# Kernel optimization log

Measured on AMD Instinct MI355X. Metric: run time of the kernel, lower is better.

## Reference

```python
import jax, jax.numpy as jnp
import numpy as np

# ---- fixed 22-node graph from the module's build_graph (clique expansion of adj_list) ----
_ADJ_LIST = [[0, 2, 5, 8, 11], [0, 1, 4, 7, 10], [0, 3, 6, 9, 12, 15],
             [9, 14, 17, 19, 21], [9, 13, 16, 18, 20]]
_N = max(max(s) for s in _ADJ_LIST) + 1  # 22
_A = np.zeros((_N, _N), dtype=np.float32)
for s in _ADJ_LIST:
    for i in range(len(s)):
        for j in range(i + 1, len(s)):
            _A[s[i], s[j]] = 1.0
            _A[s[j], s[i]] = 1.0
_deg = _A.sum(axis=1)
_dinv = 1.0 / np.sqrt(np.maximum(_deg, 1.0))
A_HAT = jnp.asarray(_dinv[:, None] * _A * _dinv[None, :])  # D^{-1/2} A D^{-1/2}, DGL norm='both'

SEQ_LEN = 100
HID = 3


def setup_inputs() -> dict:
    key = jax.random.key(0)
    ks = jax.random.split(key, 9)
    B, IN = 16384, 32
    s_in = 1.0 / np.sqrt(IN)
    s_h = 1.0 / np.sqrt(HID)
    return {
        "x": jax.random.normal(ks[0], (B, IN), jnp.float32),
        "w_r_W": jax.random.normal(ks[1], (IN, HID), jnp.float32) * s_in,
        "w_r_b": jax.random.normal(ks[2], (HID,), jnp.float32) * s_in,
        "w_z_W": jax.random.normal(ks[3], (IN, HID), jnp.float32) * s_in,
        "w_z_b": jax.random.normal(ks[4], (HID,), jnp.float32) * s_in,
        "w_h_W": jax.random.normal(ks[5], (IN, HID), jnp.float32) * s_in,
        "w_h_b": jax.random.normal(ks[6], (HID,), jnp.float32) * s_in,
        "gcn_W": jax.random.normal(ks[7], (HID, HID), jnp.float32) * s_h,
        "gcn_b": jax.random.normal(ks[8], (HID,), jnp.float32) * s_h,
    }


def reference(x, w_r_W, w_r_b, w_z_W, w_z_b, w_h_W, w_h_b, gcn_W, gcn_b):
    B = x.shape[0]
    # input projections are constant across timesteps and nodes -> compute once, broadcast
    xr = (x @ w_r_W + w_r_b)[:, None, :]  # (B,1,H)
    xz = (x @ w_z_W + w_z_b)[:, None, :]
    xh = (x @ w_h_W + w_h_b)[:, None, :]

    def step(h, _):
        # GraphConv: symmetric-normalized aggregation, then linear + bias
        gh = jnp.einsum('nm,bmh->bnh', A_HAT, h) @ gcn_W + gcn_b  # (B,N,H)
        r = jax.nn.sigmoid(xr + gh)
        z = jax.nn.sigmoid(xz + gh)
        h_tilde = jnp.tanh(xh + r * gh)
        h_new = (1.0 - z) * h + z * h_tilde
        return h_new, h_new

    h0 = jnp.zeros((B, _N, HID), x.dtype)
    _, hs = jax.lax.scan(step, h0, None, length=SEQ_LEN)  # (T,B,N,H)
    out = jnp.transpose(hs, (1, 0, 2, 3)).reshape(B, -1)  # (B, T*N*H)
    return out
```

## Files before the change

### kernel.cpp

```cpp
#include <hip/hip_runtime.h>


#define TPB 64
#define REP 4
#define RPW 16
#define NGRP (16384 / TPB)
#define GRID (NGRP * REP)
#define T_TOTAL 100
#define SCH 10
#define NCHUNK (T_TOTAL / SCH)
#define ROW_F4 (SCH * 66 / 4)
#define STG_STRIDE (SCH * 9 + 1)
#define STG_SZ (TPB * STG_STRIDE)
#define F4_PER_REP (RPW * ROW_F4)
#define GITERS ((F4_PER_REP + TPB - 1) / TPB)

#if __has_builtin(__builtin_amdgcn_exp2f)
#define EXP2F __builtin_amdgcn_exp2f
#else
#define EXP2F exp2f
#endif
#if __has_builtin(__builtin_amdgcn_rcpf)
#define RCPF __builtin_amdgcn_rcpf
#else
#define RCPF(x) (1.0f / (x))
#endif

static __device__ __forceinline__ float fast_sigmoid(float x) {
    float e = EXP2F(-1.44269504f * x);
    return RCPF(1.0f + e);
}
static __device__ __forceinline__ float fast_tanh(float x) {
    float e = EXP2F(2.88539008f * x);
    return 1.0f - 2.0f * RCPF(1.0f + e);
}

__global__ __launch_bounds__(TPB) void gcgru_kernel(
    const float* __restrict__ x,
    const float* __restrict__ w_r_W, const float* __restrict__ w_r_b,
    const float* __restrict__ w_z_W, const float* __restrict__ w_z_b,
    const float* __restrict__ w_h_W, const float* __restrict__ w_h_b,
    const float* __restrict__ gcn_W, const float* __restrict__ gcn_b,
    float* __restrict__ out)
{
    __shared__ float wS[297];
    __shared__ float gwS[9];
    __shared__ float gbS[3];
    __shared__ unsigned int tabS[ROW_F4];
    __shared__ float stage[STG_SZ];

    const int tid = threadIdx.x;
    const int rep = blockIdx.x & (REP - 1);
    const int b0  = (blockIdx.x >> 2) * TPB;
    const int row0 = rep * RPW;

    for (int i = tid; i < 96; i += TPB) {
        wS[i]       = w_r_W[i];
        wS[96 + i]  = w_z_W[i];
        wS[192 + i] = w_h_W[i];
    }
    if (tid < 3) {
        wS[288 + tid] = w_r_b[tid];
        wS[291 + tid] = w_z_b[tid];
        wS[294 + tid] = w_h_b[tid];
        gbS[tid] = gcn_b[tid];
    }
    if (tid < 9) gwS[tid] = gcn_W[tid];
    {
        static const unsigned char cls3[66] = {
            0,1,2, 3,4,5, 3,4,5, 6,7,8, 3,4,5, 3,4,5, 6,7,8, 3,4,5, 3,4,5,
            0,1,2, 3,4,5, 3,4,5, 6,7,8, 3,4,5, 3,4,5, 6,7,8, 3,4,5, 3,4,5,
            3,4,5, 3,4,5, 3,4,5, 3,4,5
        };
        for (int j4 = tid; j4 < ROW_F4; j4 += TPB) {
            unsigned int w = 0;
            #pragma unroll
            for (int u = 0; u < 4; ++u) {
                int jj = 4 * j4 + u;
                int tl = jj / 66;
                int k  = jj - 66 * tl;
                w |= (unsigned int)(tl * 9 + cls3[k]) << (8 * u);
            }
            tabS[j4] = w;
        }
    }

    float xv[32];
    {
        const float4* xp = reinterpret_cast<const float4*>(x + (size_t)(b0 + tid) * 32);
        #pragma unroll
        for (int i = 0; i < 8; ++i) {
            float4 v = xp[i];
            xv[4*i+0] = v.x; xv[4*i+1] = v.y; xv[4*i+2] = v.z; xv[4*i+3] = v.w;
        }
    }
    float xr[3], xz[3], xh[3];
    #pragma unroll
    for (int j = 0; j < 3; ++j) { xr[j] = wS[288+j]; xz[j] = wS[291+j]; xh[j] = wS[294+j]; }
    #pragma unroll
    for (int i = 0; i < 32; ++i) {
        float xi = xv[i];
        #pragma unroll
        for (int j = 0; j < 3; ++j) {
            xr[j] = fmaf(xi, wS[i*3+j],       xr[j]);
            xz[j] = fmaf(xi, wS[96 + i*3+j],  xz[j]);
            xh[j] = fmaf(xi, wS[192 + i*3+j], xh[j]);
        }
    }

    float W9[9], gb3[3];
    #pragma unroll
    for (int i = 0; i < 9; ++i) W9[i] = gwS[i];
    #pragma unroll
    for (int j = 0; j < 3; ++j) gb3[j] = gbS[j];

    const float M00 = 0.0769230769f;
    const float M01 = 1.1094003925f;
    const float M02 = 0.4961389384f;
    const float M10 = 0.1386750491f;
    const float M11 = 0.75f;
    const float M20 = 0.2480694691f;
    const float M22 = 0.6f;

    float h[9];
    #pragma unroll
    for (int i = 0; i < 9; ++i) h[i] = 0.0f;

    float4* out4 = reinterpret_cast<float4*>(out);

    for (int chunk = 0; chunk < NCHUNK; ++chunk) {
        float* stw = stage + tid * STG_STRIDE;

        #pragma unroll
        for (int s = 0; s < SCH; ++s) {
            float mh[9], gh[9];
            #pragma unroll
            for (int j = 0; j < 3; ++j) {
                mh[j]     = M00 * h[j] + M01 * h[3+j] + M02 * h[6+j];
                mh[3 + j] = M10 * h[j] + M11 * h[3+j];
                mh[6 + j] = M20 * h[j] + M22 * h[6+j];
            }
            #pragma unroll
            for (int c = 0; c < 3; ++c)
                #pragma unroll
                for (int j = 0; j < 3; ++j)
                    gh[c*3+j] = gb3[j] + mh[c*3+0]*W9[j] + mh[c*3+1]*W9[3+j] + mh[c*3+2]*W9[6+j];
            #pragma unroll
            for (int c = 0; c < 3; ++c) {
                #pragma unroll
                for (int j = 0; j < 3; ++j) {
                    float g  = gh[c*3+j];
                    float r  = fast_sigmoid(xr[j] + g);
                    float z  = fast_sigmoid(xz[j] + g);
                    float ht = fast_tanh(xh[j] + r * g);
                    float hv = h[c*3+j];
                    h[c*3+j] = hv + z * (ht - hv);
                }
            }
            #pragma unroll
            for (int q = 0; q < 9; ++q) stw[s*9 + q] = h[q];
        }


        const int cbase = chunk * ROW_F4;
        for (int i = 0; i < GITERS; ++i) {
            int f = i * TPB + tid;
            if (f < F4_PER_REP) {
                int rl = f / ROW_F4;
                int j4 = f - rl * ROW_F4;
                int r  = row0 + rl;
                unsigned int tw = tabS[j4];
                const float* row = stage + r * STG_STRIDE;
                float4 v;
                v.x = row[tw & 255u];
                v.y = row[(tw >> 8)  & 255u];
                v.z = row[(tw >> 16) & 255u];
                v.w = row[tw >> 24];
                out4[(size_t)(b0 + r) * 1650 + cbase + j4] = v;
            }
        }
    }
}

extern "C" void kernel_launch(void* const* d_in, const int* in_sizes, int n_in,
                              void* d_out, int out_size, void* d_ws, size_t ws_size,
                              hipStream_t stream) {
    const float* xp     = (const float*)d_in[0];
    const float* w_r_W  = (const float*)d_in[1];
    const float* w_r_b  = (const float*)d_in[2];
    const float* w_z_W  = (const float*)d_in[3];
    const float* w_z_b  = (const float*)d_in[4];
    const float* w_h_W  = (const float*)d_in[5];
    const float* w_h_b  = (const float*)d_in[6];
    const float* gcn_W  = (const float*)d_in[7];
    const float* gcn_b  = (const float*)d_in[8];
    float* outp = (float*)d_out;

    gcgru_kernel<<<GRID, TPB, 0, stream>>>(xp, w_r_W, w_r_b, w_z_W, w_z_b,
                                           w_h_W, w_h_b, gcn_W, gcn_b, outp);
}
```

Baseline: 497.7 us.

## Split into compact-state compute kernel and separate gather-expand kernel via workspace

The fused kernel is split in two when enough workspace is available. The first kernel runs the recurrence once per batch row, with no 4x replication, and writes a compact padded 12-float record per timestep to workspace. The second kernel expands that record into the full 22-node output through a shared-memory gather table. This removes the redundant recurrence work done by the replicated blocks, at the cost of an extra ~79MB workspace round trip and a second launch.

New measurement: 581.1 us. +16.8%, slower.

```diff
diff --git a/kernel.cpp b/kernel.cpp
--- a/kernel.cpp
+++ b/kernel.cpp
@@ -1,19 +1,31 @@
 #include <hip/hip_runtime.h>
 
 
-#define TPB 64
-#define REP 4
-#define RPW 16
-#define NGRP (16384 / TPB)
-#define GRID (NGRP * REP)
+#define TPB1 64
+#define GRID1 (16384 / TPB1)
 #define T_TOTAL 100
 #define SCH 10
 #define NCHUNK (T_TOTAL / SCH)
-#define ROW_F4 (SCH * 66 / 4)
-#define STG_STRIDE (SCH * 9 + 1)
-#define STG_SZ (TPB * STG_STRIDE)
-#define F4_PER_REP (RPW * ROW_F4)
-#define GITERS ((F4_PER_REP + TPB - 1) / TPB)
+#define REC 12
+#define ROWF (T_TOTAL * REC)
+#define ROWF4 (ROWF / 4)
+#define CH_F4 (SCH * REC / 4)
+#define K1_ITERS 30
+
+#define TPB2 256
+#define BPB2 16
+#define GRID2 (16384 / BPB2)
+#define OUT_ROW_F4 1650
+#define OUT_ELEMS 6600
+
+#define FREP 4
+#define FRPW 16
+#define FGRID (16384 / TPB1 * FREP)
+#define FROW_F4 (SCH * 66 / 4)
+#define FSTRIDE (SCH * 9 + 1)
+#define FSTG (TPB1 * FSTRIDE)
+#define F4_PER_REP (FRPW * FROW_F4)
+#define FGITERS ((F4_PER_REP + TPB1 - 1) / TPB1)
 
 #if __has_builtin(__builtin_amdgcn_exp2f)
 #define EXP2F __builtin_amdgcn_exp2f
@@ -35,85 +47,50 @@
     return 1.0f - 2.0f * RCPF(1.0f + e);
 }
 
-__global__ __launch_bounds__(TPB) void gcgru_kernel(
-    const float* __restrict__ x,
-    const float* __restrict__ w_r_W, const float* __restrict__ w_r_b,
-    const float* __restrict__ w_z_W, const float* __restrict__ w_z_b,
-    const float* __restrict__ w_h_W, const float* __restrict__ w_h_b,
-    const float* __restrict__ gcn_W, const float* __restrict__ gcn_b,
-    float* __restrict__ out)
-{
-    __shared__ float wS[297];
-    __shared__ float gwS[9];
-    __shared__ float gbS[3];
-    __shared__ unsigned int tabS[ROW_F4];
-    __shared__ float stage[STG_SZ];
-
-    const int tid = threadIdx.x;
-    const int rep = blockIdx.x & (REP - 1);
-    const int b0  = (blockIdx.x >> 2) * TPB;
-    const int row0 = rep * RPW;
-
-    for (int i = tid; i < 96; i += TPB) {
-        wS[i]       = w_r_W[i];
-        wS[96 + i]  = w_z_W[i];
-        wS[192 + i] = w_h_W[i];
-    }
-    if (tid < 3) {
-        wS[288 + tid] = w_r_b[tid];
-        wS[291 + tid] = w_z_b[tid];
-        wS[294 + tid] = w_h_b[tid];
-        gbS[tid] = gcn_b[tid];
-    }
-    if (tid < 9) gwS[tid] = gcn_W[tid];
-    {
-        static const unsigned char cls3[66] = {
-            0,1,2, 3,4,5, 3,4,5, 6,7,8, 3,4,5, 3,4,5, 6,7,8, 3,4,5, 3,4,5,
-            0,1,2, 3,4,5, 3,4,5, 6,7,8, 3,4,5, 3,4,5, 6,7,8, 3,4,5, 3,4,5,
-            3,4,5, 3,4,5, 3,4,5, 3,4,5
-        };
-        for (int j4 = tid; j4 < ROW_F4; j4 += TPB) {
-            unsigned int w = 0;
-            #pragma unroll
-            for (int u = 0; u < 4; ++u) {
-                int jj = 4 * j4 + u;
-                int tl = jj / 66;
-                int k  = jj - 66 * tl;
-                w |= (unsigned int)(tl * 9 + cls3[k]) << (8 * u);
-            }
-            tabS[j4] = w;
-        }
-    }
-
+__device__ const unsigned char d_cls3[66] = {
+    0,1,2, 3,4,5, 3,4,5, 6,7,8, 3,4,5, 3,4,5, 6,7,8, 3,4,5, 3,4,5,
+    0,1,2, 3,4,5, 3,4,5, 6,7,8, 3,4,5, 3,4,5, 6,7,8, 3,4,5, 3,4,5,
+    3,4,5, 3,4,5, 3,4,5, 3,4,5
+};
+
+struct GruConsts {
+    float xr[3], xz[3], xh[3];
+    float W9[9], gb3[3];
+};
+
+static __device__ __forceinline__ void load_consts_and_project(
+    const float* __restrict__ x, int b,
+    const float* __restrict__ wS,
+    const float* __restrict__ gwS, const float* __restrict__ gbS,
+    GruConsts& C)
+{
     float xv[32];
-    {
-        const float4* xp = reinterpret_cast<const float4*>(x + (size_t)(b0 + tid) * 32);
-        #pragma unroll
-        for (int i = 0; i < 8; ++i) {
-            float4 v = xp[i];
-            xv[4*i+0] = v.x; xv[4*i+1] = v.y; xv[4*i+2] = v.z; xv[4*i+3] = v.w;
-        }
-    }
-    float xr[3], xz[3], xh[3];
-    #pragma unroll
-    for (int j = 0; j < 3; ++j) { xr[j] = wS[288+j]; xz[j] = wS[291+j]; xh[j] = wS[294+j]; }
+    const float4* xp = reinterpret_cast<const float4*>(x + (size_t)b * 32);
+    #pragma unroll
+    for (int i = 0; i < 8; ++i) {
+        float4 v = xp[i];
+        xv[4*i+0] = v.x; xv[4*i+1] = v.y; xv[4*i+2] = v.z; xv[4*i+3] = v.w;
+    }
+    #pragma unroll
+    for (int j = 0; j < 3; ++j) { C.xr[j] = wS[288+j]; C.xz[j] = wS[291+j]; C.xh[j] = wS[294+j]; }
     #pragma unroll
     for (int i = 0; i < 32; ++i) {
         float xi = xv[i];
         #pragma unroll
         for (int j = 0; j < 3; ++j) {
-            xr[j] = fmaf(xi, wS[i*3+j],       xr[j]);
-            xz[j] = fmaf(xi, wS[96 + i*3+j],  xz[j]);
-            xh[j] = fmaf(xi, wS[192 + i*3+j], xh[j]);
-        }
-    }
-
-    float W9[9], gb3[3];
-    #pragma unroll
-    for (int i = 0; i < 9; ++i) W9[i] = gwS[i];
-    #pragma unroll
-    for (int j = 0; j < 3; ++j) gb3[j] = gbS[j];
-
+            C.xr[j] = fmaf(xi, wS[i*3+j],       C.xr[j]);
+            C.xz[j] = fmaf(xi, wS[96 + i*3+j],  C.xz[j]);
+            C.xh[j] = fmaf(xi, wS[192 + i*3+j], C.xh[j]);
+        }
+    }
+    #pragma unroll
+    for (int i = 0; i < 9; ++i) C.W9[i] = gwS[i];
+    #pragma unroll
+    for (int j = 0; j < 3; ++j) C.gb3[j] = gbS[j];
+}
+
+static __device__ __forceinline__ void gru_step(float* __restrict__ h, const GruConsts& C)
+{
     const float M00 = 0.0769230769f;
     const float M01 = 1.1094003925f;
     const float M02 = 0.4961389384f;
@@ -122,61 +99,203 @@
     const float M20 = 0.2480694691f;
     const float M22 = 0.6f;
 
+    float mh[9], gh[9];
+    #pragma unroll
+    for (int j = 0; j < 3; ++j) {
+        mh[j]     = M00 * h[j] + M01 * h[3+j] + M02 * h[6+j];
+        mh[3 + j] = M10 * h[j] + M11 * h[3+j];
+        mh[6 + j] = M20 * h[j] + M22 * h[6+j];
+    }
+    #pragma unroll
+    for (int c = 0; c < 3; ++c)
+        #pragma unroll
+        for (int j = 0; j < 3; ++j)
+            gh[c*3+j] = C.gb3[j] + mh[c*3+0]*C.W9[j] + mh[c*3+1]*C.W9[3+j] + mh[c*3+2]*C.W9[6+j];
+    #pragma unroll
+    for (int c = 0; c < 3; ++c) {
+        #pragma unroll
+        for (int j = 0; j < 3; ++j) {
+            float g  = gh[c*3+j];
+            float r  = fast_sigmoid(C.xr[j] + g);
+            float z  = fast_sigmoid(C.xz[j] + g);
+            float ht = fast_tanh(C.xh[j] + r * g);
+            float hv = h[c*3+j];
+            h[c*3+j] = hv + z * (ht - hv);
+        }
+    }
+}
+
+static __device__ __forceinline__ void stage_weights(
+    int tid, int stride,
+    const float* __restrict__ w_r_W, const float* __restrict__ w_r_b,
+    const float* __restrict__ w_z_W, const float* __restrict__ w_z_b,
+    const float* __restrict__ w_h_W, const float* __restrict__ w_h_b,
+    const float* __restrict__ gcn_W, const float* __restrict__ gcn_b,
+    float* __restrict__ wS, float* __restrict__ gwS, float* __restrict__ gbS)
+{
+    for (int i = tid; i < 96; i += stride) {
+        wS[i]       = w_r_W[i];
+        wS[96 + i]  = w_z_W[i];
+        wS[192 + i] = w_h_W[i];
+    }
+    if (tid < 3) {
+        wS[288 + tid] = w_r_b[tid];
+        wS[291 + tid] = w_z_b[tid];
+        wS[294 + tid] = w_h_b[tid];
+        gbS[tid] = gcn_b[tid];
+    }
+    if (tid < 9) gwS[tid] = gcn_W[tid];
+}
+
+__global__ __launch_bounds__(TPB1) void gcgru_compute(
+    const float* __restrict__ x,
+    const float* __restrict__ w_r_W, const float* __restrict__ w_r_b,
+    const float* __restrict__ w_z_W, const float* __restrict__ w_z_b,
+    const float* __restrict__ w_h_W, const float* __restrict__ w_h_b,
+    const float* __restrict__ gcn_W, const float* __restrict__ gcn_b,
+    float* __restrict__ compact)
+{
+    __shared__ float wS[297];
+    __shared__ float gwS[9];
+    __shared__ float gbS[3];
+    __shared__ float stage[TPB1 * SCH * REC];
+
+    const int tid = threadIdx.x;
+    const int b0  = blockIdx.x * TPB1;
+
+    stage_weights(tid, TPB1, w_r_W, w_r_b, w_z_W, w_z_b, w_h_W, w_h_b,
+                  gcn_W, gcn_b, wS, gwS, gbS);
+
+    GruConsts C;
+    load_consts_and_project(x, b0 + tid, wS, gwS, gbS, C);
+
     float h[9];
     #pragma unroll
     for (int i = 0; i < 9; ++i) h[i] = 0.0f;
 
+    float4* cmp4 = reinterpret_cast<float4*>(compact);
+
+    for (int chunk = 0; chunk < NCHUNK; ++chunk) {
+        float* stw = stage + tid * (SCH * REC);
+
+        #pragma unroll
+        for (int s = 0; s < SCH; ++s) {
+            gru_step(h, C);
+            #pragma unroll
+            for (int q = 0; q < 9; ++q) stw[s*REC + q] = h[q];
+            stw[s*REC + 9] = 0.0f; stw[s*REC + 10] = 0.0f; stw[s*REC + 11] = 0.0f;
+        }
+
+        const int cbase = chunk * CH_F4;
+        #pragma unroll
+        for (int i = 0; i < K1_ITERS; ++i) {
+            int f  = i * TPB1 + tid;
+            int rl = f / CH_F4;
+            int j4 = f - rl * CH_F4;
+            const float4* srow = reinterpret_cast<const float4*>(stage + rl * (SCH * REC));
+            cmp4[(size_t)(b0 + rl) * ROWF4 + cbase + j4] = srow[j4];
+        }
+    }
+}
+
+__global__ __launch_bounds__(TPB2) void gcgru_expand(
+    const float* __restrict__ compact,
+    float* __restrict__ out)
+{
+    __shared__ unsigned short tabE[OUT_ELEMS];
+
+    const int tid = threadIdx.x;
+    const int b0  = blockIdx.x * BPB2;
+
+    for (int jj = tid; jj < OUT_ELEMS; jj += TPB2) {
+        int t = jj / 66;
+        int k = jj - 66 * t;
+        tabE[jj] = (unsigned short)(t * REC + d_cls3[k]);
+    }
+    __syncthreads();
+
     float4* out4 = reinterpret_cast<float4*>(out);
 
+    for (int r = 0; r < BPB2; ++r) {
+        const float* cp = compact + (size_t)(b0 + r) * ROWF;
+        float4* orow = out4 + (size_t)(b0 + r) * OUT_ROW_F4;
+        for (int j4 = tid; j4 < OUT_ROW_F4; j4 += TPB2) {
+            int jj = 4 * j4;
+            float4 v;
+            v.x = cp[tabE[jj + 0]];
+            v.y = cp[tabE[jj + 1]];
+            v.z = cp[tabE[jj + 2]];
+            v.w = cp[tabE[jj + 3]];
+            orow[j4] = v;
+        }
+    }
+}
+
+__global__ __launch_bounds__(TPB1) void gcgru_fused(
+    const float* __restrict__ x,
+    const float* __restrict__ w_r_W, const float* __restrict__ w_r_b,
+    const float* __restrict__ w_z_W, const float* __restrict__ w_z_b,
+    const float* __restrict__ w_h_W, const float* __restrict__ w_h_b,
+    const float* __restrict__ gcn_W, const float* __restrict__ gcn_b,
+    float* __restrict__ out)
+{
+    __shared__ float wS[297];
+    __shared__ float gwS[9];
+    __shared__ float gbS[3];
+    __shared__ unsigned int tabS[FROW_F4];
+    __shared__ float stage[FSTG];
+
+    const int tid = threadIdx.x;
+    const int rep = blockIdx.x & (FREP - 1);
+    const int b0  = (blockIdx.x >> 2) * TPB1;
+    const int row0 = rep * FRPW;
+
+    stage_weights(tid, TPB1, w_r_W, w_r_b, w_z_W, w_z_b, w_h_W, w_h_b,
+                  gcn_W, gcn_b, wS, gwS, gbS);
+    for (int j4 = tid; j4 < FROW_F4; j4 += TPB1) {
+        unsigned int w = 0;
+        #pragma unroll
+        for (int u = 0; u < 4; ++u) {
+            int jj = 4 * j4 + u;
+            int tl = jj / 66;
+            int k  = jj - 66 * tl;
+            w |= (unsigned int)(tl * 9 + d_cls3[k]) << (8 * u);
+        }
+        tabS[j4] = w;
+    }
+
+    GruConsts C;
+    load_consts_and_project(x, b0 + tid, wS, gwS, gbS, C);
+
+    float h[9];
+    #pragma unroll
+    for (int i = 0; i < 9; ++i) h[i] = 0.0f;
+
+    float4* out4 = reinterpret_cast<float4*>(out);
+
     for (int chunk = 0; chunk < NCHUNK; ++chunk) {
-        float* stw = stage + tid * STG_STRIDE;
-
+        float* stw = stage + tid * FSTRIDE;
         #pragma unroll
         for (int s = 0; s < SCH; ++s) {
-            float mh[9], gh[9];
-            #pragma unroll
-            for (int j = 0; j < 3; ++j) {
-                mh[j]     = M00 * h[j] + M01 * h[3+j] + M02 * h[6+j];
-                mh[3 + j] = M10 * h[j] + M11 * h[3+j];
-                mh[6 + j] = M20 * h[j] + M22 * h[6+j];
-            }
-            #pragma unroll
-            for (int c = 0; c < 3; ++c)
-                #pragma unroll
-                for (int j = 0; j < 3; ++j)
-                    gh[c*3+j] = gb3[j] + mh[c*3+0]*W9[j] + mh[c*3+1]*W9[3+j] + mh[c*3+2]*W9[6+j];
-            #pragma unroll
-            for (int c = 0; c < 3; ++c) {
-                #pragma unroll
-                for (int j = 0; j < 3; ++j) {
-                    float g  = gh[c*3+j];
-                    float r  = fast_sigmoid(xr[j] + g);
-                    float z  = fast_sigmoid(xz[j] + g);
-                    float ht = fast_tanh(xh[j] + r * g);
-                    float hv = h[c*3+j];
-                    h[c*3+j] = hv + z * (ht - hv);
-                }
-            }
+            gru_step(h, C);
             #pragma unroll
             for (int q = 0; q < 9; ++q) stw[s*9 + q] = h[q];
         }
-
-
-        const int cbase = chunk * ROW_F4;
-        for (int i = 0; i < GITERS; ++i) {
-            int f = i * TPB + tid;
+        const int cbase = chunk * FROW_F4;
+        for (int i = 0; i < FGITERS; ++i) {
+            int f = i * TPB1 + tid;
             if (f < F4_PER_REP) {
-                int rl = f / ROW_F4;
-                int j4 = f - rl * ROW_F4;
+                int rl = f / FROW_F4;
+                int j4 = f - rl * FROW_F4;
                 int r  = row0 + rl;
                 unsigned int tw = tabS[j4];
-                const float* row = stage + r * STG_STRIDE;
+                const float* row = stage + r * FSTRIDE;
                 float4 v;
                 v.x = row[tw & 255u];
                 v.y = row[(tw >> 8)  & 255u];
                 v.z = row[(tw >> 16) & 255u];
                 v.w = row[tw >> 24];
-                out4[(size_t)(b0 + r) * 1650 + cbase + j4] = v;
+                out4[(size_t)(b0 + r) * OUT_ROW_F4 + cbase + j4] = v;
             }
         }
     }
@@ -196,6 +315,14 @@
     const float* gcn_b  = (const float*)d_in[8];
     float* outp = (float*)d_out;
 
-    gcgru_kernel<<<GRID, TPB, 0, stream>>>(xp, w_r_W, w_r_b, w_z_W, w_z_b,
-                                           w_h_W, w_h_b, gcn_W, gcn_b, outp);
-}
+    const size_t need = (size_t)16384 * ROWF * sizeof(float);
+    if (ws_size >= need && d_ws != nullptr) {
+        float* compact = (float*)d_ws;
+        gcgru_compute<<<GRID1, TPB1, 0, stream>>>(xp, w_r_W, w_r_b, w_z_W, w_z_b,
+                                                  w_h_W, w_h_b, gcn_W, gcn_b, compact);
+        gcgru_expand<<<GRID2, TPB2, 0, stream>>>(compact, outp);
+    } else {
+        gcgru_fused<<<FGRID, TPB1, 0, stream>>>(xp, w_r_W, w_r_b, w_z_W, w_z_b,
+                                                w_h_W, w_h_b, gcn_W, gcn_b, outp);
+    }
+}
```
